# Optimization experiments

Measured on AMD Instinct MI355X. Metric: run time of the kernel, lower is better.

Reference implementation:

```python
import jax, jax.numpy as jnp
import numpy as np
import math

NHEAD = 8
IOU_THR = 0.2
COS_THR = 0.2


def _build_mask(segments, q):
    # segments: [bz, Lq, 2] (center, length); q: [bz, Lq, d]
    c, l = segments[..., 0], segments[..., 1]
    s, e = c - l / 2, c + l / 2  # ml2se: midpoint-length -> start-end
    inter = jnp.clip(jnp.minimum(e[:, :, None], e[:, None, :])
                     - jnp.maximum(s[:, :, None], s[:, None, :]), 0.0)
    union = l[:, :, None] + l[:, None, :] - inter
    iou = inter / union  # [bz, Lq, Lq]
    qn = q / jnp.maximum(jnp.linalg.norm(q, axis=-1, keepdims=True), 1e-8)
    cos = jnp.einsum('bid,bjd->bij', qn, qn)
    Lq = q.shape[1]
    adj = jnp.broadcast_to(jnp.eye(Lq, dtype=bool), iou.shape)
    adj = jnp.where(iou <= IOU_THR, True, adj)   # adj_matrix[iou<=0.2]=1
    adj = jnp.where(cos <= COS_THR, False, adj)  # adj_matrix[cos<=0.2]=0
    return ~adj  # True = masked


def setup_inputs() -> dict:
    key = jax.random.key(0)
    ks = jax.random.split(key, 8)
    Lq, bz, d = 1024, 8, 512
    bound = 1.0 / math.sqrt(d)
    query = jax.random.normal(ks[0], (Lq, bz, d), jnp.float32)
    segments = jax.random.uniform(ks[1], (bz, Lq, 2), jnp.float32)
    Wq = jax.random.uniform(ks[2], (d, d), jnp.float32, -bound, bound)
    bq = jax.random.uniform(ks[3], (d,), jnp.float32, -bound, bound)
    Wk = jax.random.uniform(ks[4], (d, d), jnp.float32, -bound, bound)
    bk = jax.random.uniform(ks[5], (d,), jnp.float32, -bound, bound)
    Wv = jax.random.uniform(ks[6], (d, d), jnp.float32, -bound, bound)
    bv = jax.random.uniform(ks[7], (d,), jnp.float32, -bound, bound)
    return dict(query=query, segments=segments, Wq=Wq, bq=bq, Wk=Wk, bk=bk,
                Wv=Wv, bv=bv)


def reference(query, segments, Wq, bq, Wk, bk, Wv, bv):
    Lq, bz, d = query.shape
    dh = d // NHEAD
    h = jnp.transpose(query, (1, 0, 2))  # [bz, Lq, d]
    mask = _build_mask(segments, h)      # [bz, Lq, Lq], bool
    Q = (h @ Wq.T + bq).reshape(bz, Lq, NHEAD, dh)
    K = (h @ Wk.T + bk).reshape(bz, Lq, NHEAD, dh)
    V = (h @ Wv.T + bv).reshape(bz, Lq, NHEAD, dh)
    scores = jnp.einsum('bihd,bjhd->bhij', Q, K) / math.sqrt(dh)
    scores = jnp.where(mask[:, None, :, :], -jnp.inf, scores)
    attn = jax.nn.softmax(scores, axis=-1)
    out = jnp.einsum('bhij,bjhd->bihd', attn, V).reshape(bz, Lq, d) + h
    return jnp.transpose(out, (1, 0, 2))  # [Lq, bz, d]
```

## Files before the change

kernel.cpp:

```cpp
#include <hip/hip_runtime.h>
#include <math.h>

#define LQ 1024
#define BZ 8
#define D  512
#define NH 8
#define DH 64
#define IOU_THR 0.2f
#define COS_THR 0.2f
#define NEG (-1e30f)
#define FIXCAP 16384

typedef short bf16x8 __attribute__((ext_vector_type(8)));
typedef float f32x4  __attribute__((ext_vector_type(4)));

#define MFMA16(a, b, cacc) __builtin_amdgcn_mfma_f32_16x16x32_bf16(a, b, cacc, 0, 0, 0)

__device__ inline unsigned short f2bf(float x) {
    union { float f; unsigned int u; } v; v.f = x;
    unsigned int r = v.u + 0x7FFF + ((v.u >> 16) & 1);
    return (unsigned short)(r >> 16);
}

__global__ __launch_bounds__(256) void prep_kernel(const float* __restrict__ query,
                                                   const float* __restrict__ Wq,
                                                   const float* __restrict__ Wk,
                                                   const float* __restrict__ Wv,
                                                   unsigned short* __restrict__ hi,
                                                   unsigned short* __restrict__ Wb,
                                                   float* __restrict__ rnorm) {
    int blk = blockIdx.x, tid = threadIdx.x;
    if (blk < 2048) {
        int w = tid >> 6, lane = tid & 63;
        int row = blk * 4 + w;
        int b = row >> 10, i = row & 1023;
        const float* src = query + ((size_t)i * BZ + b) * D + lane * 8;
        float4 v0 = *(const float4*)src;
        float4 v1 = *(const float4*)(src + 4);
        uint4 pk;
        pk.x = (unsigned)f2bf(v0.x) | ((unsigned)f2bf(v0.y) << 16);
        pk.y = (unsigned)f2bf(v0.z) | ((unsigned)f2bf(v0.w) << 16);
        pk.z = (unsigned)f2bf(v1.x) | ((unsigned)f2bf(v1.y) << 16);
        pk.w = (unsigned)f2bf(v1.z) | ((unsigned)f2bf(v1.w) << 16);
        *(uint4*)(hi + (size_t)row * D + lane * 8) = pk;
        float ss = v0.x * v0.x + v0.y * v0.y + v0.z * v0.z + v0.w * v0.w
                 + v1.x * v1.x + v1.y * v1.y + v1.z * v1.z + v1.w * v1.w;
        #pragma unroll
        for (int s = 1; s < 64; s <<= 1) ss += __shfl_xor(ss, s);
        if (lane == 0) rnorm[row] = 1.0f / fmaxf(sqrtf(ss), 1e-8f);
    } else {
        int t = (blk - 2048) * 256 + tid;
        int mat = t >> 16;
        int off = (t & 65535) * 4;
        const float* src = (mat == 0) ? Wq : (mat == 1) ? Wk : Wv;
        float4 v = *(const float4*)(src + off);
        uint2 p;
        p.x = (unsigned)f2bf(v.x) | ((unsigned)f2bf(v.y) << 16);
        p.y = (unsigned)f2bf(v.z) | ((unsigned)f2bf(v.w) << 16);
        *(uint2*)(Wb + (size_t)mat * D * D + off) = p;
    }
}

__global__ __launch_bounds__(256) void gemm_kernel(const unsigned short* __restrict__ hi,
                                                   const unsigned short* __restrict__ Wb,
                                                   const float* __restrict__ rnorm,
                                                   const float* __restrict__ segments,
                                                   const float* __restrict__ bq,
                                                   const float* __restrict__ bk,
                                                   const float* __restrict__ bv,
                                                   unsigned char* __restrict__ mask,
                                                   unsigned char* __restrict__ summ,
                                                   int* __restrict__ fix_cnt,
                                                   unsigned int* __restrict__ fix_list,
                                                   unsigned short* __restrict__ Qb,
                                                   unsigned short* __restrict__ Kb,
                                                   unsigned short* __restrict__ Vt) {
    __shared__ __align__(16) char SMEM[35072];
    __shared__ float4 iSE[128], jSE[128];
    __shared__ int summ_lds[8][2], summ_t_lds[8][2];
    short* const As0 = (short*)SMEM;
    short* const As1 = As0 + 4096;
    short* const Bs0 = As1 + 4096;
    short* const Bs1 = Bs0 + 4096;

    int blk = blockIdx.x, tid = threadIdx.x, w = tid >> 6, lane = tid & 63;
    int c = lane & 15, q4 = lane >> 4;
    int wr = w >> 1, wc = w & 1;

    bool is_qkv = blk < 768;
    const char *Asrc, *Bsrc;
    int b = 0, i0 = 0, j0 = 0, z = 0, m0 = 0, n0 = 0;
    if (is_qkv) {
        int g = (blk & 7) + 8 * ((blk >> 3) / 12);
        int inner = (blk >> 3) % 12;
        z = inner >> 2;
        m0 = g * 128;
        n0 = (inner & 3) * 128;
        Asrc = (const char*)(hi + (size_t)m0 * D);
        Bsrc = (const char*)(Wb + (size_t)z * D * D + (size_t)n0 * D);
    } else {
        int x = blk - 768;
        b = x & 7;
        int t = x >> 3;
        int it = 0;
        while (t >= 8 - it) { t -= 8 - it; it++; }
        int jt = it + t;
        i0 = it * 128; j0 = jt * 128;
        Asrc = (const char*)(hi + ((size_t)b * LQ + i0) * D);
        Bsrc = (const char*)(hi + ((size_t)b * LQ + j0) * D);
        if (tid < 16) {
            summ_lds[tid >> 1][tid & 1] = 0;
            summ_t_lds[tid >> 1][tid & 1] = 0;
        }
    }

    int lrow = lane >> 2;
    int gl   = (lane & 3) ^ ((lane >> 3) & 3);
    size_t goff = (size_t)lrow * 1024 + (size_t)gl * 16;
    int lds_off = lrow * 64 + (lane & 3) * 16;

    uint4 ra[2], rb[2];
    #pragma unroll
    for (int m = 0; m < 2; m++) {
        int n = 2 * w + m;
        ra[m] = *(const uint4*)(Asrc + (size_t)n * 16384 + goff);
        rb[m] = *(const uint4*)(Bsrc + (size_t)n * 16384 + goff);
    }
    #pragma unroll
    for (int m = 0; m < 2; m++) {
        int n = 2 * w + m;
        *(uint4*)((char*)As0 + n * 1024 + lds_off) = ra[m];
        *(uint4*)((char*)Bs0 + n * 1024 + lds_off) = rb[m];
    }
    __syncthreads();

    f32x4 acc[4][4] = {};
    int rswz = (c >> 1) & 3;
    for (int k = 0; k < 16; k++) {
        short* Ac = (k & 1) ? As1 : As0;
        short* Bc = (k & 1) ? Bs1 : Bs0;
        if (k < 15) {
            size_t kb = (size_t)(k + 1) * 64;
            #pragma unroll
            for (int m = 0; m < 2; m++) {
                int n = 2 * w + m;
                ra[m] = *(const uint4*)(Asrc + kb + (size_t)n * 16384 + goff);
                rb[m] = *(const uint4*)(Bsrc + kb + (size_t)n * 16384 + goff);
            }
        }
        bf16x8 af[4], bf[4];
        #pragma unroll
        for (int f = 0; f < 4; f++) {
            af[f] = *(const bf16x8*)&Ac[(wr * 64 + f * 16 + c) * 32 + (q4 ^ rswz) * 8];
            bf[f] = *(const bf16x8*)&Bc[(wc * 64 + f * 16 + c) * 32 + (q4 ^ rswz) * 8];
        }
        #pragma unroll
        for (int fr = 0; fr < 4; fr++)
            #pragma unroll
            for (int fc = 0; fc < 4; fc++)
                acc[fr][fc] = MFMA16(af[fr], bf[fc], acc[fr][fc]);
        if (k < 15) {
            short* An = (k & 1) ? As0 : As1;
            short* Bn = (k & 1) ? Bs0 : Bs1;
            #pragma unroll
            for (int m = 0; m < 2; m++) {
                int n = 2 * w + m;
                *(uint4*)((char*)An + n * 1024 + lds_off) = ra[m];
                *(uint4*)((char*)Bn + n * 1024 + lds_off) = rb[m];
            }
        }
        __syncthreads();
    }

    if (is_qkv) {
        const float* bias = (z == 0) ? bq : (z == 1) ? bk : bv;
        #pragma unroll
        for (int fr = 0; fr < 4; fr++)
            #pragma unroll
            for (int r = 0; r < 4; r++) {
                int row = wr * 64 + fr * 16 + q4 * 4 + r;
                char* rbase = SMEM + row * 272 + (row >> 3) * 16;
                #pragma unroll
                for (int fc = 0; fc < 4; fc++) {
                    int col = wc * 64 + fc * 16 + c;
                    *(unsigned short*)(rbase + col * 2) =
                        f2bf(acc[fr][fc][r] + bias[n0 + col]);
                }
            }
        __syncthreads();
        int bb = m0 >> 10, ib = m0 & 1023;
        if (z < 2) {
            unsigned short* dst = (z == 0) ? Qb : Kb;
            #pragma unroll
            for (int it2 = 0; it2 < 8; it2++) {
                int idx = it2 * 256 + tid;
                int row = idx >> 4, cg = idx & 15;
                uint4 v = *(const uint4*)(SMEM + row * 272 + (row >> 3) * 16 + cg * 16);
                int n = n0 + cg * 8;
                int hh = n >> 6, dh = n & 63;
                *(uint4*)(dst + (((size_t)bb * NH + hh) * LQ + ib + row) * DH + dh) = v;
            }
        } else {
            #pragma unroll
            for (int it2 = 0; it2 < 8; it2++) {
                int idx = it2 * 256 + tid;
                int rowg = idx & 15, colI = idx >> 4;
                union { unsigned short s[8]; uint4 v; } u;
                char* gbase = SMEM + rowg * 16;
                #pragma unroll
                for (int rr = 0; rr < 8; rr++)
                    u.s[rr] = *(const unsigned short*)(gbase + (rowg * 8 + rr) * 272 + colI * 2);
                int n = n0 + colI;
                int hh = n >> 6, dh = n & 63;
                *(uint4*)(Vt + (((size_t)bb * NH + hh) * DH + dh) * LQ + ib + rowg * 8) = u.v;
            }
        }
    } else {
        const float2* seg2 = (const float2*)(segments + (size_t)b * LQ * 2);
        const float* rn = rnorm + b * LQ;
        if (tid < 128) {
            float2 cl = seg2[i0 + tid];
            iSE[tid] = make_float4(cl.x - cl.y * 0.5f, cl.x + cl.y * 0.5f, cl.y, rn[i0 + tid]);
        } else {
            float2 cl = seg2[j0 + tid - 128];
            jSE[tid - 128] = make_float4(cl.x - cl.y * 0.5f, cl.x + cl.y * 0.5f, cl.y, rn[j0 + tid - 128]);
        }
        __syncthreads();

        bool offdiag = (i0 != j0);
        unsigned char* mbase = mask + ((size_t)b << 20);
        int anyT[4] = {0, 0, 0, 0};
        #pragma unroll
        for (int fr = 0; fr < 4; fr++) {
            int anyun = 0;
            unsigned int tpack[4] = {0, 0, 0, 0};
            #pragma unroll
            for (int r = 0; r < 4; r++) {
                int il = wr * 64 + fr * 16 + q4 * 4 + r;
                int i = i0 + il;
                float4 I = iSE[il];
                #pragma unroll
                for (int fc = 0; fc < 4; fc++) {
                    int jl = wc * 64 + fc * 16 + c;
                    int j = j0 + jl;
                    float4 J = jSE[jl];
                    float cosv = acc[fr][fc][r] * I.w * J.w;
                    if (fabsf(cosv - COS_THR) < 1.5e-3f) {
                        int idx = atomicAdd(fix_cnt, 1);
                        if (idx < FIXCAP)
                            fix_list[idx] = ((unsigned int)b << 20) | ((unsigned int)i << 10) | j;
                    }
                    float inter = fmaxf(fminf(I.y, J.y) - fmaxf(I.x, J.x), 0.0f);
                    float uni   = I.z + J.z - inter;
                    float iou   = inter / uni;
                    bool adj = ((iou <= IOU_THR) || (i == j)) && (cosv > COS_THR);
                    mbase[(size_t)i * LQ + j] = adj ? 0 : 1;
                    tpack[fc] |= (adj ? 0u : 1u) << (8 * r);
                    anyun |= adj ? 1 : 0;
                    anyT[fc] |= adj ? 1 : 0;
                }
            }
            if (anyun) atomicOr(&summ_lds[wr * 4 + fr][wc], 1);
            if (offdiag) {
                int ibase = i0 + wr * 64 + fr * 16 + q4 * 4;
                #pragma unroll
                for (int fc = 0; fc < 4; fc++) {
                    int j = j0 + wc * 64 + fc * 16 + c;
                    *(unsigned int*)&mbase[(size_t)j * LQ + ibase] = tpack[fc];
                }
            }
        }
        if (offdiag) {
            #pragma unroll
            for (int fc = 0; fc < 4; fc++)
                if (anyT[fc]) atomicOr(&summ_t_lds[wc * 4 + fc][wr], 1);
        }
        __syncthreads();
        if (tid < 16) {
            int lit = tid >> 1, ljt = tid & 1;
            summ[((size_t)b * 64 + (i0 >> 4) + lit) * 16 + (j0 >> 6) + ljt] =
                summ_lds[lit][ljt] ? 1 : 0;
            if (offdiag)
                summ[((size_t)b * 64 + (j0 >> 4) + lit) * 16 + (i0 >> 6) + ljt] =
                    summ_t_lds[lit][ljt] ? 1 : 0;
        }
    }
}

__global__ __launch_bounds__(64) void fixup_kernel(const float* __restrict__ query,
                                                   const float* __restrict__ rnorm,
                                                   const float* __restrict__ segments,
                                                   const int* __restrict__ fix_cnt,
                                                   const unsigned int* __restrict__ fix_list,
                                                   unsigned char* __restrict__ mask,
                                                   unsigned char* __restrict__ summ) {
    int cnt = *fix_cnt; if (cnt > FIXCAP) cnt = FIXCAP;
    int lane = threadIdx.x;
    for (int e = blockIdx.x; e < cnt; e += gridDim.x) {
        unsigned int pk = fix_list[e];
        int b = pk >> 20, i = (pk >> 10) & 1023, j = pk & 1023;
        const float* hri = query + ((size_t)i * BZ + b) * D;
        const float* hrj = query + ((size_t)j * BZ + b) * D;
        double dd = 0.0;
        #pragma unroll
        for (int k = 0; k < D / 64; k++)
            dd += (double)hri[k * 64 + lane] * (double)hrj[k * 64 + lane];
        #pragma unroll
        for (int s = 1; s < 64; s <<= 1) dd += __shfl_xor(dd, s);
        if (lane == 0) {
            float rni = rnorm[b * LQ + i], rnj = rnorm[b * LQ + j];
            float cosv = (float)(dd * (double)rni * (double)rnj);
            const float* seg = segments + (size_t)b * LQ * 2;
            float ci = seg[i * 2], li = seg[i * 2 + 1];
            float cj = seg[j * 2], lj = seg[j * 2 + 1];
            float si = ci - li * 0.5f, ei = ci + li * 0.5f;
            float sj = cj - lj * 0.5f, ej = cj + lj * 0.5f;
            float inter = fmaxf(fminf(ei, ej) - fmaxf(si, sj), 0.0f);
            float iou = inter / (li + lj - inter);
            bool adj = ((iou <= IOU_THR) || (i == j)) && (cosv > COS_THR);
            unsigned char mv = adj ? 0 : 1;
            mask[((size_t)b * LQ + i) * LQ + j] = mv;
            mask[((size_t)b * LQ + j) * LQ + i] = mv;
            if (adj) {
                summ[((size_t)b * 64 + (i >> 4)) * 16 + (j >> 6)] = 1;
                summ[((size_t)b * 64 + (j >> 4)) * 16 + (i >> 6)] = 1;
            }
        }
    }
}

__global__ __launch_bounds__(256) void attn_kernel(const unsigned short* __restrict__ Qb,
                                                   const unsigned short* __restrict__ Kb,
                                                   const unsigned short* __restrict__ Vt,
                                                   const unsigned char* __restrict__ mask,
                                                   const unsigned char* __restrict__ summ,
                                                   const float* __restrict__ query,
                                                   float* __restrict__ out) {
    int tid = threadIdx.x;
    int w = tid >> 6, lane = tid & 63;
    int c = lane & 15, q4 = lane >> 4;
    int hh = blockIdx.y, b = blockIdx.z;
    int i0 = blockIdx.x * 64 + w * 16;
    size_t bh = (size_t)b * NH + hh;

    __shared__ unsigned short p_lds[4][16][72];

    const unsigned short* Qrow = Qb + (bh * LQ + i0 + c) * DH;
    bf16x8 qa0 = *(const bf16x8*)(Qrow + q4 * 8);
    bf16x8 qa1 = *(const bf16x8*)(Qrow + 32 + q4 * 8);

    f32x4 O[4] = {};
    float m_r[4] = {NEG, NEG, NEG, NEG};
    float l_r[4] = {0.f, 0.f, 0.f, 0.f};

    const unsigned short* Kbase = Kb + bh * LQ * DH;
    const unsigned short* Vbase = Vt + bh * DH * LQ;
    const unsigned char*  mbase = mask + ((size_t)b * LQ + i0) * LQ;
    const unsigned char*  srow  = summ + ((size_t)b * 64 + (i0 >> 4)) * 16;

    for (int jt = 0; jt < 16; jt++) {
        if (!srow[jt]) continue;
        int j0 = jt * 64;
        f32x4 S[4] = {};
        #pragma unroll
        for (int cb = 0; cb < 4; cb++) {
            const unsigned short* krow = Kbase + (size_t)(j0 + cb * 16 + c) * DH;
            bf16x8 kf0 = *(const bf16x8*)(krow + q4 * 8);
            bf16x8 kf1 = *(const bf16x8*)(krow + 32 + q4 * 8);
            S[cb] = MFMA16(qa0, kf0, S[cb]);
            S[cb] = MFMA16(qa1, kf1, S[cb]);
        }
        float p[4][4];
        float tmax[4] = {NEG, NEG, NEG, NEG};
        #pragma unroll
        for (int cb = 0; cb < 4; cb++)
            #pragma unroll
            for (int r = 0; r < 4; r++) {
                float sc = S[cb][r] * 0.125f;
                unsigned char mm = mbase[(size_t)(q4 * 4 + r) * LQ + j0 + cb * 16 + c];
                sc = mm ? NEG : sc;
                p[cb][r] = sc;
                tmax[r] = fmaxf(tmax[r], sc);
            }
        #pragma unroll
        for (int r = 0; r < 4; r++) {
            float v = tmax[r];
            v = fmaxf(v, __shfl_xor(v, 1));
            v = fmaxf(v, __shfl_xor(v, 2));
            v = fmaxf(v, __shfl_xor(v, 4));
            v = fmaxf(v, __shfl_xor(v, 8));
            tmax[r] = v;
        }
        float rsum[4];
        #pragma unroll
        for (int r = 0; r < 4; r++) {
            float mn = fmaxf(m_r[r], tmax[r]);
            float alpha = __expf(m_r[r] - mn);
            m_r[r] = mn;
            l_r[r] *= alpha;
            #pragma unroll
            for (int cb2 = 0; cb2 < 4; cb2++) O[cb2][r] *= alpha;
            float s0 = 0.f;
            #pragma unroll
            for (int cb = 0; cb < 4; cb++) {
                float e = __expf(p[cb][r] - mn);
                p[cb][r] = e;
                s0 += e;
            }
            rsum[r] = s0;
        }
        #pragma unroll
        for (int r = 0; r < 4; r++) {
            float v = rsum[r];
            v += __shfl_xor(v, 1);
            v += __shfl_xor(v, 2);
            v += __shfl_xor(v, 4);
            v += __shfl_xor(v, 8);
            l_r[r] += v;
        }
        #pragma unroll
        for (int cb = 0; cb < 4; cb++)
            #pragma unroll
            for (int r = 0; r < 4; r++)
                p_lds[w][q4 * 4 + r][cb * 16 + c] = f2bf(p[cb][r]);
        #pragma unroll
        for (int s = 0; s < 2; s++) {
            bf16x8 pf = *(const bf16x8*)&p_lds[w][c][s * 32 + q4 * 8];
            #pragma unroll
            for (int cb = 0; cb < 4; cb++) {
                bf16x8 vf = *(const bf16x8*)(Vbase + (size_t)(cb * 16 + c) * LQ + j0 + s * 32 + q4 * 8);
                O[cb] = MFMA16(pf, vf, O[cb]);
            }
        }
    }
    #pragma unroll
    for (int r = 0; r < 4; r++) {
        int i = i0 + q4 * 4 + r;
        float inv = 1.0f / l_r[r];
        #pragma unroll
        for (int cb = 0; cb < 4; cb++) {
            int col = hh * 64 + cb * 16 + c;
            size_t oidx = ((size_t)i * BZ + b) * D + col;
            out[oidx] = O[cb][r] * inv + query[oidx];
        }
    }
}

extern "C" void kernel_launch(void* const* d_in, const int* in_sizes, int n_in,
                              void* d_out, int out_size, void* d_ws, size_t ws_size,
                              hipStream_t stream) {
    const float* query    = (const float*)d_in[0];
    const float* segments = (const float*)d_in[1];
    const float* Wq = (const float*)d_in[2];
    const float* bq = (const float*)d_in[3];
    const float* Wk = (const float*)d_in[4];
    const float* bk = (const float*)d_in[5];
    const float* Wv = (const float*)d_in[6];
    const float* bv = (const float*)d_in[7];
    float* out = (float*)d_out;

    const size_t NTOK = (size_t)BZ * LQ;
    char* ws = (char*)d_ws;
    unsigned short* hbuf  = (unsigned short*)ws;   ws += NTOK * D * 2;
    unsigned short* Qb    = (unsigned short*)ws;   ws += NTOK * D * 2;
    unsigned short* Kb    = (unsigned short*)ws;   ws += NTOK * D * 2;
    unsigned short* Vt    = (unsigned short*)ws;   ws += NTOK * D * 2;
    unsigned short* Wb    = (unsigned short*)ws;   ws += (size_t)3 * D * D * 2;
    float*          rnorm = (float*)ws;            ws += NTOK * 4;
    unsigned char*  mask  = (unsigned char*)ws;    ws += (size_t)BZ * LQ * LQ;
    unsigned char*  summ  = (unsigned char*)ws;    ws += 8192;
    int*            fix_cnt = (int*)ws;            ws += 64;
    unsigned int*   fix_list = (unsigned int*)ws;

    hipMemsetAsync(fix_cnt, 0, 64, stream);
    prep_kernel<<<2816, 256, 0, stream>>>(query, Wq, Wk, Wv, hbuf, Wb, rnorm);
    gemm_kernel<<<1056, 256, 0, stream>>>(hbuf, Wb, rnorm, segments, bq, bk, bv,
                                          mask, summ, fix_cnt, fix_list, Qb, Kb, Vt);
    fixup_kernel<<<64, 64, 0, stream>>>(query, rnorm, segments, fix_cnt, fix_list, mask, summ);
    attn_kernel<<<dim3(LQ / 64, NH, BZ), 256, 0, stream>>>(Qb, Kb, Vt, mask, summ, query, out);
}
```

Baseline: 150.1 us.

## Load GEMM MFMA fragments directly from global memory, dropping LDS staging

The GEMM main loop stops staging A and B tiles through double-buffered shared memory with block barriers. Each wave now loads its MFMA operand fragments straight from global memory into registers, with a two-stage register prefetch. This removes LDS writes, LDS reads and the per-step __syncthreads. In exchange, tiles shared between waves are fetched from global/L2 twice, and each lane issues narrower strided row reads, which raises global traffic and latency exposure.

```diff
diff --git a/kernel.cpp b/kernel.cpp
--- a/kernel.cpp
+++ b/kernel.cpp
@@ -78,10 +78,6 @@
     __shared__ __align__(16) char SMEM[35072];
     __shared__ float4 iSE[128], jSE[128];
     __shared__ int summ_lds[8][2], summ_t_lds[8][2];
-    short* const As0 = (short*)SMEM;
-    short* const As1 = As0 + 4096;
-    short* const Bs0 = As1 + 4096;
-    short* const Bs1 = Bs0 + 4096;
 
     int blk = blockIdx.x, tid = threadIdx.x, w = tid >> 6, lane = tid & 63;
     int c = lane & 15, q4 = lane >> 4;
@@ -114,62 +110,46 @@
         }
     }
 
-    int lrow = lane >> 2;
-    int gl   = (lane & 3) ^ ((lane >> 3) & 3);
-    size_t goff = (size_t)lrow * 1024 + (size_t)gl * 16;
-    int lds_off = lrow * 64 + (lane & 3) * 16;
-
-    uint4 ra[2], rb[2];
+    const char* Aptr[4];
+    const char* Bptr[4];
     #pragma unroll
-    for (int m = 0; m < 2; m++) {
-        int n = 2 * w + m;
-        ra[m] = *(const uint4*)(Asrc + (size_t)n * 16384 + goff);
-        rb[m] = *(const uint4*)(Bsrc + (size_t)n * 16384 + goff);
-    }
+    for (int f = 0; f < 4; f++) {
+        Aptr[f] = Asrc + (size_t)(wr * 64 + f * 16 + c) * 1024 + q4 * 16;
+        Bptr[f] = Bsrc + (size_t)(wc * 64 + f * 16 + c) * 1024 + q4 * 16;
+    }
+
+    f32x4 acc[4][4] = {};
+    bf16x8 a0[4], b0[4], a1[4], b1[4];
     #pragma unroll
-    for (int m = 0; m < 2; m++) {
-        int n = 2 * w + m;
-        *(uint4*)((char*)As0 + n * 1024 + lds_off) = ra[m];
-        *(uint4*)((char*)Bs0 + n * 1024 + lds_off) = rb[m];
-    }
-    __syncthreads();
-
-    f32x4 acc[4][4] = {};
-    int rswz = (c >> 1) & 3;
-    for (int k = 0; k < 16; k++) {
-        short* Ac = (k & 1) ? As1 : As0;
-        short* Bc = (k & 1) ? Bs1 : Bs0;
-        if (k < 15) {
-            size_t kb = (size_t)(k + 1) * 64;
-            #pragma unroll
-            for (int m = 0; m < 2; m++) {
-                int n = 2 * w + m;
-                ra[m] = *(const uint4*)(Asrc + kb + (size_t)n * 16384 + goff);
-                rb[m] = *(const uint4*)(Bsrc + kb + (size_t)n * 16384 + goff);
-            }
-        }
-        bf16x8 af[4], bf[4];
-        #pragma unroll
-        for (int f = 0; f < 4; f++) {
-            af[f] = *(const bf16x8*)&Ac[(wr * 64 + f * 16 + c) * 32 + (q4 ^ rswz) * 8];
-            bf[f] = *(const bf16x8*)&Bc[(wc * 64 + f * 16 + c) * 32 + (q4 ^ rswz) * 8];
+    for (int f = 0; f < 4; f++) {
+        a0[f] = *(const bf16x8*)Aptr[f];
+        b0[f] = *(const bf16x8*)Bptr[f];
+    }
+    for (int k = 0; k < 16; k += 2) {
+        if (k + 1 < 16) {
+            #pragma unroll
+            for (int f = 0; f < 4; f++) {
+                a1[f] = *(const bf16x8*)(Aptr[f] + (k + 1) * 64);
+                b1[f] = *(const bf16x8*)(Bptr[f] + (k + 1) * 64);
+            }
         }
         #pragma unroll
         for (int fr = 0; fr < 4; fr++)
             #pragma unroll
             for (int fc = 0; fc < 4; fc++)
-                acc[fr][fc] = MFMA16(af[fr], bf[fc], acc[fr][fc]);
-        if (k < 15) {
-            short* An = (k & 1) ? As0 : As1;
-            short* Bn = (k & 1) ? Bs0 : Bs1;
-            #pragma unroll
-            for (int m = 0; m < 2; m++) {
-                int n = 2 * w + m;
-                *(uint4*)((char*)An + n * 1024 + lds_off) = ra[m];
-                *(uint4*)((char*)Bn + n * 1024 + lds_off) = rb[m];
-            }
-        }
-        __syncthreads();
+                acc[fr][fc] = MFMA16(a0[fr], b0[fc], acc[fr][fc]);
+        if (k + 2 < 16) {
+            #pragma unroll
+            for (int f = 0; f < 4; f++) {
+                a0[f] = *(const bf16x8*)(Aptr[f] + (k + 2) * 64);
+                b0[f] = *(const bf16x8*)(Bptr[f] + (k + 2) * 64);
+            }
+        }
+        #pragma unroll
+        for (int fr = 0; fr < 4; fr++)
+            #pragma unroll
+            for (int fc = 0; fc < 4; fc++)
+                acc[fr][fc] = MFMA16(a1[fr], b1[fc], acc[fr][fc]);
     }
 
     if (is_qkv) {
```

Result: slower. 191.9 us (+27.9%).
